# Optimization experiments

Hardware: AMD Instinct MI355X
Metric: run time of the kernel (lower is better)

## Reference

```python
import jax, jax.numpy as jnp
import numpy as np

EPSILON = 1000000000.0
N_HEADS = 8
N_UNITS = 512
D_K = N_UNITS // N_HEADS  # 64
B, S = 2, 2048


def setup_inputs() -> dict:
    key = jax.random.key(0)
    ks = jax.random.split(key, 12)
    k_init = 1.0 / np.sqrt(N_UNITS)
    u = lambda k, shape: jax.random.uniform(k, shape, jnp.float32, -k_init, k_init)
    return {
        "query": jax.random.normal(ks[0], (B, S, N_UNITS), jnp.float32),
        "key": jax.random.normal(ks[1], (B, S, N_UNITS), jnp.float32),
        "value": jax.random.normal(ks[2], (B, S, N_UNITS), jnp.float32),
        "mask": jnp.ones((B, S, S), jnp.float32),
        # Stacked per-head projection weights, [H, D, d_k] (x @ W), biases [H, d_k]
        "Wq": u(ks[3], (N_HEADS, N_UNITS, D_K)),
        "bq": u(ks[4], (N_HEADS, D_K)),
        "Wk": u(ks[5], (N_HEADS, N_UNITS, D_K)),
        "bk": u(ks[6], (N_HEADS, D_K)),
        "Wv": u(ks[7], (N_HEADS, N_UNITS, D_K)),
        "bv": u(ks[8], (N_HEADS, D_K)),
        # Output projection: x @ Wo + bo, Wo [D, D]
        "Wo": u(ks[9], (N_UNITS, N_UNITS)),
        "bo": u(ks[10], (N_UNITS,)),
    }


def reference(query, key, value, mask, Wq, bq, Wk, bk, Wv, bv, Wo, bo):
    # Batched over heads: q/k/v projections -> [B, H, S, d_k]
    q = jnp.einsum("bsd,hdk->bhsk", query, Wq) + bq[None, :, None, :]
    k = jnp.einsum("bsd,hdk->bhsk", key, Wk) + bk[None, :, None, :]
    v = jnp.einsum("bsd,hdk->bhsk", value, Wv) + bv[None, :, None, :]
    # Scaled dot-product scores [B, H, S, S]
    scores = jnp.einsum("bhsk,bhtk->bhst", q, k) / jnp.sqrt(jnp.asarray(D_K, q.dtype))
    # Additive masking exactly as original: x*mask - EPS*(1-mask)
    m = mask[:, None, :, :]
    scores = scores * m - EPSILON * (1.0 - m)
    a = jax.nn.softmax(scores, axis=-1)
    ctx = jnp.einsum("bhst,bhtk->bhsk", a, v)  # [B, H, S, d_k]
    # Concatenate heads along feature dim -> [B, S, H*d_k]
    h_out = ctx.transpose(0, 2, 1, 3).reshape(query.shape[0], query.shape[1], N_UNITS)
    return h_out @ Wo + bo
```

## Files before the change

kernel.cpp:

```cpp
#include <hip/hip_runtime.h>
#include <hip/hip_bf16.h>


#define DEVI __device__ __forceinline__

typedef float f32x4 __attribute__((ext_vector_type(4)));
typedef float f32x16 __attribute__((ext_vector_type(16)));
typedef __bf16 bf16x8 __attribute__((ext_vector_type(8)));

constexpr int S  = 2048;
constexpr int D  = 512;
constexpr int H  = 8;
constexpr int DK = 64;
constexpr int BATCH = 2;
constexpr int BS = BATCH * S;

constexpr float SCALE_QK = 0.18033688011112433f;
constexpr float EPS2     = 1.4426950408889634e9f;

DEVI unsigned short f2bf(float f) {
  union { float f; unsigned u; } v; v.f = f;
  unsigned r = v.u + 0x7fffu + ((v.u >> 16) & 1u);
  return (unsigned short)(r >> 16);
}

DEVI unsigned pk2(float a, float b) {
  return (unsigned)f2bf(a) | ((unsigned)f2bf(b) << 16);
}

DEVI f32x4 mfma16(bf16x8 a, bf16x8 b, f32x4 c) {
  return __builtin_amdgcn_mfma_f32_16x16x32_bf16(a, b, c, 0, 0, 0);
}
DEVI f32x16 mfma32(bf16x8 a, bf16x8 b, f32x16 c) {
  return __builtin_amdgcn_mfma_f32_32x32x16_bf16(a, b, c, 0, 0, 0);
}

DEVI bf16x8 ldg8(const unsigned short* p) { return *(const bf16x8*)p; }

__global__ __launch_bounds__(256) void prep_w_kernel(
    const float* __restrict__ Wq, const float* __restrict__ Wk,
    const float* __restrict__ Wv, const float* __restrict__ Wo,
    unsigned short* __restrict__ Wt)
{
  __shared__ float T[64][65];
  int bid = blockIdx.x;
  int g = bid >> 6, t = bid & 63;
  int tn = t >> 3, td = t & 7;
  int n0 = tn * 64, d0 = td * 64;
  int tid = threadIdx.x;
  const float* src = (g == 0) ? Wq : (g == 1) ? Wk : (g == 2) ? Wv : Wo;

  #pragma unroll
  for (int cc = 0; cc < 4; ++cc) {
    int id = tid + cc * 256;
    int dd = id >> 4, f4 = (id & 15) * 4;
    const float* p = (g < 3)
      ? src + ((size_t)tn * D + d0 + dd) * DK + f4
      : src + (size_t)(d0 + dd) * D + n0 + f4;
    float4 x = *(const float4*)p;
    T[dd][f4 + 0] = x.x; T[dd][f4 + 1] = x.y;
    T[dd][f4 + 2] = x.z; T[dd][f4 + 3] = x.w;
  }
  __syncthreads();

  #pragma unroll
  for (int cc = 0; cc < 2; ++cc) {
    int id = tid + cc * 256;
    int nn = id >> 3, ch = (id & 7) * 8;
    unsigned short o8[8];
    #pragma unroll
    for (int j = 0; j < 8; ++j) o8[j] = f2bf(T[ch + j][nn]);
    *(uint4*)&Wt[((size_t)g * D + n0 + nn) * D + d0 + ch] = *(const uint4*)o8;
  }
}

__global__ __launch_bounds__(256) void proj_qkv_kernel(
    const float* __restrict__ query, const float* __restrict__ key,
    const float* __restrict__ value, const unsigned short* __restrict__ Wt,
    const float* __restrict__ bq, const float* __restrict__ bk, const float* __restrict__ bv,
    unsigned short* __restrict__ Qb, unsigned short* __restrict__ Kb,
    unsigned short* __restrict__ Vtb)
{
  int z = blockIdx.z;
  const float* A = (z == 0) ? query : (z == 1) ? key : value;
  const unsigned short* Bt = Wt + (size_t)z * D * D;
  const float* bias = (z == 0) ? bq : (z == 1) ? bk : bv;

  __shared__ __align__(16) unsigned short SM[2 * 128 * 72];
  unsigned short (*At)[72]    = (unsigned short(*)[72])SM;
  unsigned short (*Btile)[72] = (unsigned short(*)[72])(SM + 128 * 72);

  int tid = threadIdx.x;
  int w = tid >> 6, l = tid & 63;
  int g = l >> 4, c = l & 15;
  int wm = w >> 1, wn = w & 1;
  int m0 = blockIdx.y * 128, n0 = blockIdx.x * 128;

  f32x4 acc[4][4];
  #pragma unroll
  for (int i = 0; i < 4; ++i)
    #pragma unroll
    for (int j = 0; j < 4; ++j) acc[i][j] = f32x4{0.f, 0.f, 0.f, 0.f};

  for (int k0 = 0; k0 < D; k0 += 64) {
    __syncthreads();
    #pragma unroll
    for (int cc = 0; cc < 4; ++cc) {
      int id = tid + cc * 256;
      int row = id >> 3, ch = (id & 7) * 8;
      const float* p = A + (size_t)(m0 + row) * D + k0 + ch;
      float4 x0 = *(const float4*)p, x1 = *(const float4*)(p + 4);
      unsigned short o8[8] = { f2bf(x0.x), f2bf(x0.y), f2bf(x0.z), f2bf(x0.w),
                               f2bf(x1.x), f2bf(x1.y), f2bf(x1.z), f2bf(x1.w) };
      *(uint4*)&At[row][ch] = *(const uint4*)o8;
      *(bf16x8*)&Btile[row][ch] = ldg8(Bt + (size_t)(n0 + row) * D + k0 + ch);
    }
    __syncthreads();
    #pragma unroll
    for (int dc = 0; dc < 2; ++dc) {
      bf16x8 af[4], bv4[4];
      #pragma unroll
      for (int i = 0; i < 4; ++i)
        af[i] = *(const bf16x8*)&At[wm * 64 + i * 16 + c][dc * 32 + 8 * g];
      #pragma unroll
      for (int j = 0; j < 4; ++j)
        bv4[j] = *(const bf16x8*)&Btile[wn * 64 + j * 16 + c][dc * 32 + 8 * g];
      #pragma unroll
      for (int i = 0; i < 4; ++i)
        #pragma unroll
        for (int j = 0; j < 4; ++j)
          acc[i][j] = mfma16(af[i], bv4[j], acc[i][j]);
    }
  }

  if (z < 2) {
    #pragma unroll
    for (int i = 0; i < 4; ++i) {
      #pragma unroll
      for (int j = 0; j < 4; ++j) {
        int col = n0 + wn * 64 + j * 16 + c;
        float bb = bias[col];
        #pragma unroll
        for (int r = 0; r < 4; ++r) {
          int m = m0 + wm * 64 + i * 16 + 4 * g + r;
          float vv = acc[i][j][r] + bb;
          if (z == 0) vv *= SCALE_QK;
          unsigned short o = f2bf(vv);
          if (z == 0) Qb[(size_t)m * D + col] = o;
          else        Kb[(size_t)m * D + col] = o;
        }
      }
    }
  } else {
    __syncthreads();
    unsigned short (*Vl)[130] = (unsigned short(*)[130])SM;
    #pragma unroll
    for (int i = 0; i < 4; ++i)
      #pragma unroll
      for (int j = 0; j < 4; ++j) {
        int col = wn * 64 + j * 16 + c;
        float bb = bias[n0 + col];
        #pragma unroll
        for (int r = 0; r < 4; ++r)
          Vl[wm * 64 + i * 16 + 4 * g + r][col] = f2bf(acc[i][j][r] + bb);
      }
    __syncthreads();
    int b_ = m0 >> 11, s0b = m0 & 2047;
    #pragma unroll
    for (int it = 0; it < 8; ++it) {
      int id = tid + it * 256;
      int nl = id >> 4, chm = (id & 15) * 8;
      unsigned short o8[8];
      #pragma unroll
      for (int jj = 0; jj < 8; ++jj) o8[jj] = Vl[chm + jj][nl];
      *(uint4*)(Vtb + ((size_t)b_ * D + n0 + nl) * S + s0b + chm) = *(const uint4*)o8;
    }
  }
}

__global__ __launch_bounds__(256) void proj_o_kernel(
    const unsigned short* __restrict__ Ctx, const unsigned short* __restrict__ Bt,
    const float* __restrict__ bo, float* __restrict__ out)
{
  __shared__ __align__(16) unsigned short At[64][72];
  __shared__ __align__(16) unsigned short Btile[64][72];

  int tid = threadIdx.x;
  int w = tid >> 6, l = tid & 63;
  int g = l >> 4, c = l & 15;
  int wm = w >> 1, wn = w & 1;
  int m0 = blockIdx.y * 64, n0 = blockIdx.x * 64;

  f32x4 acc[2][2];
  #pragma unroll
  for (int i = 0; i < 2; ++i)
    #pragma unroll
    for (int j = 0; j < 2; ++j) acc[i][j] = f32x4{0.f, 0.f, 0.f, 0.f};

  for (int k0 = 0; k0 < D; k0 += 64) {
    __syncthreads();
    #pragma unroll
    for (int cc = 0; cc < 2; ++cc) {
      int id = tid + cc * 256;
      int row = id >> 3, ch = (id & 7) * 8;
      *(bf16x8*)&At[row][ch]    = ldg8(Ctx + (size_t)(m0 + row) * D + k0 + ch);
      *(bf16x8*)&Btile[row][ch] = ldg8(Bt  + (size_t)(n0 + row) * D + k0 + ch);
    }
    __syncthreads();
    #pragma unroll
    for (int dc = 0; dc < 2; ++dc) {
      bf16x8 af[2], bv4[2];
      #pragma unroll
      for (int i = 0; i < 2; ++i)
        af[i] = *(const bf16x8*)&At[wm * 32 + i * 16 + c][dc * 32 + 8 * g];
      #pragma unroll
      for (int j = 0; j < 2; ++j)
        bv4[j] = *(const bf16x8*)&Btile[wn * 32 + j * 16 + c][dc * 32 + 8 * g];
      #pragma unroll
      for (int i = 0; i < 2; ++i)
        #pragma unroll
        for (int j = 0; j < 2; ++j)
          acc[i][j] = mfma16(af[i], bv4[j], acc[i][j]);
    }
  }

  #pragma unroll
  for (int i = 0; i < 2; ++i)
    #pragma unroll
    for (int j = 0; j < 2; ++j) {
      int col = n0 + wn * 32 + j * 16 + c;
      float bb = bo[col];
      #pragma unroll
      for (int r = 0; r < 4; ++r) {
        int m = m0 + wm * 32 + i * 16 + 4 * g + r;
        out[(size_t)m * D + col] = acc[i][j][r] + bb;
      }
    }
}

__global__ __launch_bounds__(256) void attn_kernel(
    const unsigned short* __restrict__ Qb, const unsigned short* __restrict__ Kb,
    const unsigned short* __restrict__ Vtb, const float* __restrict__ mask,
    unsigned short* __restrict__ Ctx)
{
  __shared__ __align__(16) unsigned short Kt[64 * 64];
  __shared__ __align__(16) unsigned short Vt[64 * 64];
  __shared__ __align__(16) unsigned short Ol[4][32][72];

  int tid = threadIdx.x;
  int wid = tid >> 6, l = tid & 63;
  int ql = l & 31, half = l >> 5;
  int bh = blockIdx.y, b = bh >> 3, h = bh & 7;
  int q0 = blockIdx.x * 128 + wid * 32;
  int q = q0 + ql;

  bf16x8 qf[4];
  #pragma unroll
  for (int t = 0; t < 4; ++t)
    qf[t] = ldg8(Qb + (size_t)(b * S + q) * D + h * DK + t * 16 + half * 8);

  float m_run = -1e30f, l_run = 0.f;
  f32x16 o0, o1;
  #pragma unroll
  for (int i = 0; i < 16; ++i) { o0[i] = 0.f; o1[i] = 0.f; }

  for (int kb = 0; kb < S; kb += 64) {
    __syncthreads();
    #pragma unroll
    for (int it = 0; it < 2; ++it) {
      int id = tid + it * 256;
      int row = id >> 3, ch = id & 7;
      int sw = ((ch * 16) ^ ((row & 7) << 4)) >> 1;
      *(bf16x8*)(Kt + row * 64 + sw) =
          ldg8(Kb + (size_t)(b * S + kb + row) * D + h * DK + ch * 8);
      *(bf16x8*)(Vt + row * 64 + sw) =
          ldg8(Vtb + ((size_t)b * D + h * DK + row) * S + kb + ch * 8);
    }
    __syncthreads();

    f32x16 s0, s1;
    #pragma unroll
    for (int i = 0; i < 16; ++i) { s0[i] = 0.f; s1[i] = 0.f; }
    #pragma unroll
    for (int t = 0; t < 4; ++t) {
      int cb = ((t * 32 + half * 16) ^ ((ql & 7) << 4)) >> 1;
      bf16x8 k0 = *(const bf16x8*)(Kt + ql * 64 + cb);
      bf16x8 k1 = *(const bf16x8*)(Kt + (32 + ql) * 64 + cb);
      s0 = mfma32(k0, qf[t], s0);
      s1 = mfma32(k1, qf[t], s1);
    }

    float y[2][16];
    const float* mrow = mask + ((size_t)b * S + q) * S + kb;
    #pragma unroll
    for (int ks = 0; ks < 2; ++ks)
      #pragma unroll
      for (int rg = 0; rg < 4; ++rg) {
        float4 mv = *(const float4*)(mrow + ks * 32 + rg * 8 + half * 4);
        float sv0 = ks ? s1[rg * 4 + 0] : s0[rg * 4 + 0];
        float sv1 = ks ? s1[rg * 4 + 1] : s0[rg * 4 + 1];
        float sv2 = ks ? s1[rg * 4 + 2] : s0[rg * 4 + 2];
        float sv3 = ks ? s1[rg * 4 + 3] : s0[rg * 4 + 3];
        y[ks][rg * 4 + 0] = fmaf(sv0, mv.x, fmaf(EPS2, mv.x, -EPS2));
        y[ks][rg * 4 + 1] = fmaf(sv1, mv.y, fmaf(EPS2, mv.y, -EPS2));
        y[ks][rg * 4 + 2] = fmaf(sv2, mv.z, fmaf(EPS2, mv.z, -EPS2));
        y[ks][rg * 4 + 3] = fmaf(sv3, mv.w, fmaf(EPS2, mv.w, -EPS2));
      }

    float mx = -1e30f;
    #pragma unroll
    for (int ks = 0; ks < 2; ++ks)
      #pragma unroll
      for (int i = 0; i < 16; ++i) mx = fmaxf(mx, y[ks][i]);
    mx = fmaxf(mx, __shfl_xor(mx, 32, 64));
    float mnew = fmaxf(m_run, mx);
    float corr = exp2f(m_run - mnew);
    m_run = mnew;

    float p[2][16];
    float rs = 0.f;
    #pragma unroll
    for (int ks = 0; ks < 2; ++ks)
      #pragma unroll
      for (int i = 0; i < 16; ++i) {
        float pe = exp2f(y[ks][i] - mnew);
        p[ks][i] = pe;
        rs += pe;
      }
    rs += __shfl_xor(rs, 32, 64);
    l_run = l_run * corr + rs;
    o0 = o0 * corr;
    o1 = o1 * corr;

    unsigned w[2][4][2], xw[2][4][2];
    #pragma unroll
    for (int ks = 0; ks < 2; ++ks)
      #pragma unroll
      for (int rg = 0; rg < 4; ++rg) {
        w[ks][rg][0] = pk2(p[ks][rg * 4 + 0], p[ks][rg * 4 + 1]);
        w[ks][rg][1] = pk2(p[ks][rg * 4 + 2], p[ks][rg * 4 + 3]);
      }
    #pragma unroll
    for (int ks = 0; ks < 2; ++ks)
      #pragma unroll
      for (int rg = 0; rg < 4; ++rg) {
        xw[ks][rg][0] = (unsigned)__shfl_xor((int)w[ks][rg][0], 32, 64);
        xw[ks][rg][1] = (unsigned)__shfl_xor((int)w[ks][rg][1], 32, 64);
      }

    bf16x8 pa[4];
    #pragma unroll
    for (int ks = 0; ks < 2; ++ks)
      #pragma unroll
      for (int sub = 0; sub < 2; ++sub) {
        unsigned u0 = half ? xw[ks][2 * sub + 1][0] : w[ks][2 * sub][0];
        unsigned u1 = half ? xw[ks][2 * sub + 1][1] : w[ks][2 * sub][1];
        unsigned u2 = half ? w[ks][2 * sub + 1][0]  : xw[ks][2 * sub][0];
        unsigned u3 = half ? w[ks][2 * sub + 1][1]  : xw[ks][2 * sub][1];
        union { unsigned u[4]; bf16x8 v; } pu;
        pu.u[0] = u0; pu.u[1] = u1; pu.u[2] = u2; pu.u[3] = u3;
        pa[ks * 2 + sub] = pu.v;
      }

    #pragma unroll
    for (int kp = 0; kp < 4; ++kp) {
      int cb = ((kp * 32 + half * 16) ^ ((ql & 7) << 4)) >> 1;
      bf16x8 v0 = *(const bf16x8*)(Vt + ql * 64 + cb);
      bf16x8 v1 = *(const bf16x8*)(Vt + (32 + ql) * 64 + cb);
      o0 = mfma32(v0, pa[kp], o0);
      o1 = mfma32(v1, pa[kp], o1);
    }
  }

  float inv = 1.0f / l_run;
  #pragma unroll
  for (int i = 0; i < 16; ++i) {
    int dr = (i & 3) + 8 * (i >> 2) + 4 * half;
    Ol[wid][ql][dr]      = f2bf(o0[i] * inv);
    Ol[wid][ql][32 + dr] = f2bf(o1[i] * inv);
  }
  #pragma unroll
  for (int it = 0; it < 4; ++it) {
    int id = l + it * 64;
    int row = id >> 3, ch = (id & 7) * 8;
    bf16x8 vv = *(const bf16x8*)&Ol[wid][row][ch];
    *(bf16x8*)(Ctx + (size_t)(b * S + q0 + row) * D + h * DK + ch) = vv;
  }
}

extern "C" void kernel_launch(void* const* d_in, const int* in_sizes, int n_in,
                              void* d_out, int out_size, void* d_ws, size_t ws_size,
                              hipStream_t stream) {
  (void)in_sizes; (void)n_in; (void)out_size; (void)ws_size;
  const float* query = (const float*)d_in[0];
  const float* key   = (const float*)d_in[1];
  const float* value = (const float*)d_in[2];
  const float* mask  = (const float*)d_in[3];
  const float* Wq    = (const float*)d_in[4];
  const float* bq    = (const float*)d_in[5];
  const float* Wk    = (const float*)d_in[6];
  const float* bk    = (const float*)d_in[7];
  const float* Wv    = (const float*)d_in[8];
  const float* bv    = (const float*)d_in[9];
  const float* Wo    = (const float*)d_in[10];
  const float* bo    = (const float*)d_in[11];
  float* out = (float*)d_out;

  char* ws = (char*)d_ws;
  unsigned short* Wt  = (unsigned short*)(ws);
  unsigned short* Qb  = (unsigned short*)(ws + 2097152);
  unsigned short* Kb  = (unsigned short*)(ws + 6291456);
  unsigned short* Vtb = (unsigned short*)(ws + 10485760);
  unsigned short* Ctx = (unsigned short*)(ws + 14680064);

  hipLaunchKernelGGL(prep_w_kernel, dim3(256), dim3(256), 0, stream,
                     Wq, Wk, Wv, Wo, Wt);
  hipLaunchKernelGGL(proj_qkv_kernel, dim3(4, 32, 3), dim3(256), 0, stream,
                     query, key, value, Wt, bq, bk, bv, Qb, Kb, Vtb);
  hipLaunchKernelGGL(attn_kernel, dim3(16, 16), dim3(256), 0, stream,
                     Qb, Kb, Vtb, mask, Ctx);
  hipLaunchKernelGGL(proj_o_kernel, dim3(8, 64), dim3(256), 0, stream,
                     Ctx, Wt + 3 * D * D, bo, out);
}
```

Measured before the change: 232.9 us.

## Split attention KV dimension across blocks with merge kernel and register prefetch

Adds a split-KV (flash-decoding style) path: the attention grid gains a z dimension over KV chunks, each block writes a partial unnormalized bf16 output plus running max and sum, and a new merge kernel combines them into Ctx. The aim is to lift the grid from 256 blocks to as many as 1024 so the GPU's compute units are better occupied. K/V tiles are also prefetched into registers one tile ahead to overlap global loads with compute, and launch bounds request 4 blocks per SM. The cost is extra partial-output traffic, an extra launch, and bf16 rounding of unnormalized partials before the merge. The split count depends on workspace size.

```diff
diff --git a/kernel.cpp b/kernel.cpp
--- a/kernel.cpp
+++ b/kernel.cpp
@@ -36,6 +36,9 @@
 }
 
 DEVI bf16x8 ldg8(const unsigned short* p) { return *(const bf16x8*)p; }
+DEVI float bf2f(unsigned short u) {
+  union { unsigned u; float f; } v; v.u = (unsigned)u << 16; return v.f;
+}
 
 __global__ __launch_bounds__(256) void prep_w_kernel(
     const float* __restrict__ Wq, const float* __restrict__ Wk,
@@ -238,10 +241,12 @@
     }
 }
 
-__global__ __launch_bounds__(256) void attn_kernel(
+__global__ __launch_bounds__(256, 4) void attn_kernel(
     const unsigned short* __restrict__ Qb, const unsigned short* __restrict__ Kb,
     const unsigned short* __restrict__ Vtb, const float* __restrict__ mask,
-    unsigned short* __restrict__ Ctx)
+    unsigned short* __restrict__ Ctx, unsigned short* __restrict__ Opart,
+    float* __restrict__ Mpart, float* __restrict__ Lpart,
+    int kvlen, int direct)
 {
   __shared__ __align__(16) unsigned short Kt[64 * 64];
   __shared__ __align__(16) unsigned short Vt[64 * 64];
@@ -251,6 +256,9 @@
   int wid = tid >> 6, l = tid & 63;
   int ql = l & 31, half = l >> 5;
   int bh = blockIdx.y, b = bh >> 3, h = bh & 7;
+  int sp = blockIdx.z;
+  int kv0 = sp * kvlen;
+  int ntiles = kvlen >> 6;
   int q0 = blockIdx.x * 128 + wid * 32;
   int q = q0 + ql;
 
@@ -264,17 +272,31 @@
   #pragma unroll
   for (int i = 0; i < 16; ++i) { o0[i] = 0.f; o1[i] = 0.f; }
 
-  for (int kb = 0; kb < S; kb += 64) {
-    __syncthreads();
-    #pragma unroll
-    for (int it = 0; it < 2; ++it) {
-      int id = tid + it * 256;
-      int row = id >> 3, ch = id & 7;
-      int sw = ((ch * 16) ^ ((row & 7) << 4)) >> 1;
-      *(bf16x8*)(Kt + row * 64 + sw) =
-          ldg8(Kb + (size_t)(b * S + kb + row) * D + h * DK + ch * 8);
-      *(bf16x8*)(Vt + row * 64 + sw) =
-          ldg8(Vtb + ((size_t)b * D + h * DK + row) * S + kb + ch * 8);
+  int srow = tid >> 3, sch = tid & 7;
+  int ssw = ((sch * 16) ^ ((srow & 7) << 4)) >> 1;
+  int srow2 = (tid + 256) >> 3, sch2 = (tid + 256) & 7;
+  int ssw2 = ((sch2 * 16) ^ ((srow2 & 7) << 4)) >> 1;
+  bf16x8 kpre0, kpre1, vpre0, vpre1;
+  {
+    kpre0 = ldg8(Kb + (size_t)(b * S + kv0 + srow) * D + h * DK + sch * 8);
+    vpre0 = ldg8(Vtb + ((size_t)b * D + h * DK + srow) * S + kv0 + sch * 8);
+    kpre1 = ldg8(Kb + (size_t)(b * S + kv0 + srow2) * D + h * DK + sch2 * 8);
+    vpre1 = ldg8(Vtb + ((size_t)b * D + h * DK + srow2) * S + kv0 + sch2 * 8);
+  }
+
+  for (int t = 0; t < ntiles; ++t) {
+    int kb = kv0 + t * 64;
+    __syncthreads();
+    *(bf16x8*)(Kt + srow * 64 + ssw)   = kpre0;
+    *(bf16x8*)(Vt + srow * 64 + ssw)   = vpre0;
+    *(bf16x8*)(Kt + srow2 * 64 + ssw2) = kpre1;
+    *(bf16x8*)(Vt + srow2 * 64 + ssw2) = vpre1;
+    if (t + 1 < ntiles) {
+      int kn = kb + 64;
+      kpre0 = ldg8(Kb + (size_t)(b * S + kn + srow) * D + h * DK + sch * 8);
+      vpre0 = ldg8(Vtb + ((size_t)b * D + h * DK + srow) * S + kn + sch * 8);
+      kpre1 = ldg8(Kb + (size_t)(b * S + kn + srow2) * D + h * DK + sch2 * 8);
+      vpre1 = ldg8(Vtb + ((size_t)b * D + h * DK + srow2) * S + kn + sch2 * 8);
     }
     __syncthreads();
 
@@ -282,12 +304,12 @@
     #pragma unroll
     for (int i = 0; i < 16; ++i) { s0[i] = 0.f; s1[i] = 0.f; }
     #pragma unroll
-    for (int t = 0; t < 4; ++t) {
-      int cb = ((t * 32 + half * 16) ^ ((ql & 7) << 4)) >> 1;
+    for (int t4 = 0; t4 < 4; ++t4) {
+      int cb = ((t4 * 32 + half * 16) ^ ((ql & 7) << 4)) >> 1;
       bf16x8 k0 = *(const bf16x8*)(Kt + ql * 64 + cb);
       bf16x8 k1 = *(const bf16x8*)(Kt + (32 + ql) * 64 + cb);
-      s0 = mfma32(k0, qf[t], s0);
-      s1 = mfma32(k1, qf[t], s1);
+      s0 = mfma32(k0, qf[t4], s0);
+      s1 = mfma32(k1, qf[t4], s1);
     }
 
     float y[2][16];
@@ -372,26 +394,73 @@
     }
   }
 
-  float inv = 1.0f / l_run;
+  float sc = direct ? (1.0f / l_run) : 1.0f;
   #pragma unroll
   for (int i = 0; i < 16; ++i) {
     int dr = (i & 3) + 8 * (i >> 2) + 4 * half;
-    Ol[wid][ql][dr]      = f2bf(o0[i] * inv);
-    Ol[wid][ql][32 + dr] = f2bf(o1[i] * inv);
+    Ol[wid][ql][dr]      = f2bf(o0[i] * sc);
+    Ol[wid][ql][32 + dr] = f2bf(o1[i] * sc);
+  }
+  if (!direct && half == 0) {
+    size_t mi = ((size_t)sp * 16 + bh) * 2048 + q;
+    Mpart[mi] = m_run;
+    Lpart[mi] = l_run;
   }
   #pragma unroll
   for (int it = 0; it < 4; ++it) {
     int id = l + it * 64;
     int row = id >> 3, ch = (id & 7) * 8;
     bf16x8 vv = *(const bf16x8*)&Ol[wid][row][ch];
-    *(bf16x8*)(Ctx + (size_t)(b * S + q0 + row) * D + h * DK + ch) = vv;
-  }
+    if (direct)
+      *(bf16x8*)(Ctx + (size_t)(b * S + q0 + row) * D + h * DK + ch) = vv;
+    else
+      *(bf16x8*)(Opart + (((size_t)sp * 16 + bh) * 2048 + q0 + row) * DK + ch) = vv;
+  }
+}
+
+template <int NSPLIT>
+__global__ __launch_bounds__(256) void attn_merge_kernel(
+    const unsigned short* __restrict__ Opart, const float* __restrict__ Mpart,
+    const float* __restrict__ Lpart, unsigned short* __restrict__ Ctx)
+{
+  int tid = blockIdx.x * 256 + threadIdx.x;
+  int chunk = tid & 7;
+  int q = (tid >> 3) & 2047;
+  int bh = tid >> 14;
+  int b = bh >> 3, h = bh & 7;
+
+  float ms[NSPLIT], ls[NSPLIT];
+  float M = -3e38f;
+  #pragma unroll
+  for (int sp = 0; sp < NSPLIT; ++sp) {
+    size_t mi = ((size_t)sp * 16 + bh) * 2048 + q;
+    ms[sp] = Mpart[mi];
+    ls[sp] = Lpart[mi];
+    M = fmaxf(M, ms[sp]);
+  }
+  float osum[8];
+  #pragma unroll
+  for (int j = 0; j < 8; ++j) osum[j] = 0.f;
+  float lsum = 0.f;
+  #pragma unroll
+  for (int sp = 0; sp < NSPLIT; ++sp) {
+    float wsp = exp2f(ms[sp] - M);
+    lsum += wsp * ls[sp];
+    bf16x8 ov = ldg8(Opart + (((size_t)sp * 16 + bh) * 2048 + q) * DK + chunk * 8);
+    #pragma unroll
+    for (int j = 0; j < 8; ++j) osum[j] += wsp * bf2f(((unsigned short*)&ov)[j]);
+  }
+  float inv = 1.0f / lsum;
+  unsigned short o8[8];
+  #pragma unroll
+  for (int j = 0; j < 8; ++j) o8[j] = f2bf(osum[j] * inv);
+  *(uint4*)(Ctx + (size_t)(b * S + q) * D + h * DK + chunk * 8) = *(const uint4*)o8;
 }
 
 extern "C" void kernel_launch(void* const* d_in, const int* in_sizes, int n_in,
                               void* d_out, int out_size, void* d_ws, size_t ws_size,
                               hipStream_t stream) {
-  (void)in_sizes; (void)n_in; (void)out_size; (void)ws_size;
+  (void)in_sizes; (void)n_in; (void)out_size;
   const float* query = (const float*)d_in[0];
   const float* key   = (const float*)d_in[1];
   const float* value = (const float*)d_in[2];
@@ -413,12 +482,27 @@
   unsigned short* Vtb = (unsigned short*)(ws + 10485760);
   unsigned short* Ctx = (unsigned short*)(ws + 14680064);
 
+  const size_t base = 18874368ull, per = 4456448ull;
+  int nsplit = (ws_size >= base + 4 * per) ? 4
+             : (ws_size >= base + 2 * per) ? 2 : 1;
+  unsigned short* Opart = (unsigned short*)(ws + base);
+  float* Mpart = (float*)(ws + base + (size_t)nsplit * 4194304);
+  float* Lpart = (float*)(ws + base + (size_t)nsplit * 4194304 + (size_t)nsplit * 131072);
+  int kvlen = S / nsplit;
+
   hipLaunchKernelGGL(prep_w_kernel, dim3(256), dim3(256), 0, stream,
                      Wq, Wk, Wv, Wo, Wt);
   hipLaunchKernelGGL(proj_qkv_kernel, dim3(4, 32, 3), dim3(256), 0, stream,
                      query, key, value, Wt, bq, bk, bv, Qb, Kb, Vtb);
-  hipLaunchKernelGGL(attn_kernel, dim3(16, 16), dim3(256), 0, stream,
-                     Qb, Kb, Vtb, mask, Ctx);
+  hipLaunchKernelGGL(attn_kernel, dim3(16, 16, nsplit), dim3(256), 0, stream,
+                     Qb, Kb, Vtb, mask, Ctx, Opart, Mpart, Lpart,
+                     kvlen, (int)(nsplit == 1));
+  if (nsplit == 4)
+    hipLaunchKernelGGL(attn_merge_kernel<4>, dim3(1024), dim3(256), 0, stream,
+                       Opart, Mpart, Lpart, Ctx);
+  else if (nsplit == 2)
+    hipLaunchKernelGGL(attn_merge_kernel<2>, dim3(1024), dim3(256), 0, stream,
+                       Opart, Mpart, Lpart, Ctx);
   hipLaunchKernelGGL(proj_o_kernel, dim3(8, 64), dim3(256), 0, stream,
                      Ctx, Wt + 3 * D * D, bo, out);
 }
```

New measurement: 213.4 us. -8.4%, faster.
